# Optimization experiments

Measured on AMD Instinct MI355X. Metric: run time of the kernel, lower is better.

The kernel has to match this reference:

```python
import jax, jax.numpy as jnp
import numpy as np

NUM_KNOTS = 10
DEGREE = 3
NUM_BASIS = NUM_KNOTS + DEGREE - 1  # 12
IN_FEATURES = 512
OUT_FEATURES = 512


def _interval_bounds():
    # t = linspace(0,1,num_knots); segment i covers [t[max(0,i-deg+1)], t[min(i+1,K-1)])
    t = np.linspace(0.0, 1.0, NUM_KNOTS, dtype=np.float32)
    idx = np.arange(NUM_BASIS)
    lower = t[np.maximum(0, idx - (DEGREE - 1))]
    upper = t[np.minimum(idx + 1, NUM_KNOTS - 1)]
    return jnp.asarray(lower), jnp.asarray(upper)


def setup_inputs() -> dict:
    key = jax.random.key(0)
    kx, kc = jax.random.split(key)
    x = jax.random.uniform(kx, (8, 2048, IN_FEATURES), dtype=jnp.float32)
    # coeffs for spline (i=out, j=in): torch indexes splines[i*in_features+j]
    coeffs = jax.random.normal(kc, (OUT_FEATURES, IN_FEATURES, NUM_BASIS), dtype=jnp.float32)
    return {"x": x, "coeffs": coeffs}


def reference(x, coeffs):
    lower, upper = _interval_bounds()  # [NUM_BASIS] each
    # piecewise-constant basis masks: [b, s, in, NUM_BASIS]
    xe = x[..., None]
    basis = ((xe >= lower) & (xe < upper)).astype(x.dtype)
    # out[b,s,i] = sum_j sum_k basis[b,s,j,k] * coeffs[i,j,k]
    return jnp.einsum("bsjk,ijk->bsi", basis, coeffs)
```

## Files before the change

### kernel.cpp

```cpp
#include <hip/hip_runtime.h>

#define MTOT 16384
#define NFEAT 512
#define KTOT 4608

typedef float f32x16 __attribute__((ext_vector_type(16)));
typedef short s16x8 __attribute__((ext_vector_type(8)));

__device__ __forceinline__ int div9(int c) { return (c * 7282) >> 16; }

#define GLDS(GP, LP) __builtin_amdgcn_global_load_lds( \
    (const __attribute__((address_space(1))) void*)(GP), \
    (__attribute__((address_space(3))) void*)(LP), 16, 0, 0)

__device__ __forceinline__ s16x8 decode_mask(unsigned msk) {
  unsigned e0 = (msk & 15u) * 0x00204081u & 0x01010101u;
  unsigned e1 = (msk >> 4)  * 0x00204081u & 0x01010101u;
  unsigned d0 = __builtin_amdgcn_perm(e0, e0, 0x0C010C00u) * 0x3F80u;
  unsigned d1 = __builtin_amdgcn_perm(e0, e0, 0x0C030C02u) * 0x3F80u;
  unsigned d2 = __builtin_amdgcn_perm(e1, e1, 0x0C010C00u) * 0x3F80u;
  unsigned d3 = __builtin_amdgcn_perm(e1, e1, 0x0C030C02u) * 0x3F80u;
  union { unsigned d[4]; s16x8 v; } u;
  u.d[0] = d0; u.d[1] = d1; u.d[2] = d2; u.d[3] = d3;
  return u.v;
}

__global__ __launch_bounds__(256) void prep(const float* __restrict__ x,
                                            const float* __restrict__ coeffs,
                                            unsigned char* __restrict__ codeT,
                                            unsigned short* __restrict__ Bmat) {
  __shared__ unsigned char segt[64][68];
  const int bx = blockIdx.x;
  const int tid = threadIdx.x;
  if (bx < 2048) {
    const int i = bx >> 2, q = bx & 3;
    const float* cb = coeffs + (size_t)i * 6144;
#pragma unroll
    for (int p = 0; p < 5; ++p) {
      int kl = p * 256 + tid;
      if (kl < 1152) {
        int k = q * 1152 + kl;
        int j = div9(k), s = k - j * 9;
        float v = cb[j * 12 + s] + cb[j * 12 + s + 1] + cb[j * 12 + s + 2];
        unsigned u = __float_as_uint(v);
        unsigned rn = (u + 0x7FFFu + ((u >> 16) & 1u)) >> 16;
        Bmat[(size_t)i * KTOT + k] = (unsigned short)rn;
      }
    }
  } else {
    const int bb = bx - 2048;
    const int mt = bb >> 3;
    const int jt = bb & 7;
    const int m0 = mt * 64;
    const float4* x4 = (const float4*)x;
    const float T1 = (float)(1.0/9.0), T2 = (float)(2.0/9.0), T3 = (float)(3.0/9.0),
                T4 = (float)(4.0/9.0), T5 = (float)(5.0/9.0), T6 = (float)(6.0/9.0),
                T7 = (float)(7.0/9.0), T8 = (float)(8.0/9.0);
#pragma unroll
    for (int it = 0; it < 4; ++it) {
      int f = it * 256 + tid;
      int m = f >> 4, jq = f & 15;
      float4 v = x4[(size_t)(m0 + m) * 128 + jt * 16 + jq];
      uchar4 sv;
      { float xv = v.x; sv.x = (unsigned char)((xv>=T1)+(xv>=T2)+(xv>=T3)+(xv>=T4)+(xv>=T5)+(xv>=T6)+(xv>=T7)+(xv>=T8)); }
      { float xv = v.y; sv.y = (unsigned char)((xv>=T1)+(xv>=T2)+(xv>=T3)+(xv>=T4)+(xv>=T5)+(xv>=T6)+(xv>=T7)+(xv>=T8)); }
      { float xv = v.z; sv.z = (unsigned char)((xv>=T1)+(xv>=T2)+(xv>=T3)+(xv>=T4)+(xv>=T5)+(xv>=T6)+(xv>=T7)+(xv>=T8)); }
      { float xv = v.w; sv.w = (unsigned char)((xv>=T1)+(xv>=T2)+(xv>=T3)+(xv>=T4)+(xv>=T5)+(xv>=T6)+(xv>=T7)+(xv>=T8)); }
      *(uchar4*)&segt[m][jq * 4] = sv;
    }
    __syncthreads();
#pragma unroll
    for (int p = 0; p < 5; ++p) {
      int u = p * 256 + tid;
      if (u < 1152) {
        int gl = u >> 4, mq = u & 15;
        int c0 = jt * 576 + gl * 8;
        int j0 = div9(c0), j1 = div9(c0 + 7);
        int j0l = j0 - jt * 64, j1l = j1 - jt * 64;
        uchar4 ob;
        unsigned char* pb = (unsigned char*)&ob;
#pragma unroll
        for (int c = 0; c < 4; ++c) {
          int m = mq * 4 + c;
          int s0 = segt[m][j0l];
          int pos0 = j0 * 9 + s0 - c0;
          unsigned code = (pos0 >= 0 && pos0 < 8) ? (1u << pos0) : 0u;
          if (j1 != j0) {
            int s1 = segt[m][j1l];
            int pos1 = j1 * 9 + s1 - c0;
            if (pos1 < 8) code |= (1u << pos1);
          }
          pb[c] = (unsigned char)code;
        }
        *(uchar4*)(codeT + (size_t)(jt * 72 + gl) * MTOT + m0 + mq * 4) = ob;
      }
    }
  }
}

__global__ __launch_bounds__(256, 2) void kan_gemm(const unsigned char* __restrict__ codeT,
                                                   const unsigned short* __restrict__ Bmat,
                                                   float* __restrict__ out) {
  __shared__ __align__(16) short Blds[2][8 * 512];
  const int tid = threadIdx.x;
  const int lane = tid & 63;
  const int wid = tid >> 6;
  const int l5 = lane & 31;
  const int lh = lane >> 5;
  const int bx = blockIdx.x;
  const int nt = bx & 7;
  const int mt = bx >> 3;
  const int m0 = mt * 256, n0 = nt * 64;

  const int s0 = 2 * wid, s1 = 2 * wid + 1;
  const unsigned short* gB0 = Bmat + (size_t)(n0 + (s0 >> 2) * 32 + l5) * KTOT + (s0 & 3) * 16 + lh * 8;
  const unsigned short* gB1 = Bmat + (size_t)(n0 + (s1 >> 2) * 32 + l5) * KTOT + (s1 & 3) * 16 + lh * 8;
  const unsigned char* gCk0 = codeT + (size_t)(0 * 2 + lh) * MTOT + m0 + wid * 64 + l5;
  const unsigned char* gCk1 = codeT + (size_t)(1 * 2 + lh) * MTOT + m0 + wid * 64 + l5;
  const unsigned char* gCk2 = codeT + (size_t)(2 * 2 + lh) * MTOT + m0 + wid * 64 + l5;
  const unsigned char* gCk3 = codeT + (size_t)(3 * 2 + lh) * MTOT + m0 + wid * 64 + l5;

  f32x16 acc[2][2] = {};
  unsigned char crA[8], crB[8];

#define LOAD_CR(CR) do { \
    CR[0] = gCk0[0];  CR[4] = gCk0[32]; \
    CR[1] = gCk1[0];  CR[5] = gCk1[32]; \
    CR[2] = gCk2[0];  CR[6] = gCk2[32]; \
    CR[3] = gCk3[0];  CR[7] = gCk3[32]; \
    gCk0 += (size_t)8 * MTOT; gCk1 += (size_t)8 * MTOT; \
    gCk2 += (size_t)8 * MTOT; gCk3 += (size_t)8 * MTOT; } while (0)

#define ISSUE_B(buf) do { \
    GLDS(gB0, &Blds[buf][0] + s0 * 512); \
    GLDS(gB1, &Blds[buf][0] + s1 * 512); \
    gB0 += 64; gB1 += 64; } while (0)

#define COMPUTE(CR, buf) do { \
    _Pragma("unroll") \
    for (int ks = 0; ks < 4; ++ks) { \
      s16x8 b0 = *(const s16x8*)&Blds[buf][(0 * 4 + ks) * 512 + lane * 8]; \
      s16x8 b1 = *(const s16x8*)&Blds[buf][(1 * 4 + ks) * 512 + lane * 8]; \
      _Pragma("unroll") \
      for (int ms = 0; ms < 2; ++ms) { \
        s16x8 a = decode_mask(CR[ms * 4 + ks]); \
        acc[ms][0] = __builtin_amdgcn_mfma_f32_32x32x16_bf16(a, b0, acc[ms][0], 0, 0, 0); \
        acc[ms][1] = __builtin_amdgcn_mfma_f32_32x32x16_bf16(a, b1, acc[ms][1], 0, 0, 0); \
      } \
    } } while (0)

  LOAD_CR(crA);
  ISSUE_B(0);
  LOAD_CR(crB);
  __syncthreads();

#pragma unroll 1
  for (int kt = 0; kt < 72; kt += 2) {
    ISSUE_B(1);
    COMPUTE(crA, 0);
    if (kt < 70) LOAD_CR(crA);
    __syncthreads();
    if (kt < 70) ISSUE_B(0);
    COMPUTE(crB, 1);
    if (kt < 70) LOAD_CR(crB);
    __syncthreads();
  }

#pragma unroll
  for (int ms = 0; ms < 2; ++ms) {
#pragma unroll
    for (int ns = 0; ns < 2; ++ns) {
      int rowbase = m0 + wid * 64 + ms * 32 + 4 * lh;
      int col = n0 + ns * 32 + l5;
      float* op = out + (size_t)rowbase * NFEAT + col;
#pragma unroll
      for (int rg = 0; rg < 16; ++rg) {
        int row_off = (rg & 3) + 8 * (rg >> 2);
        op[(size_t)row_off * NFEAT] = acc[ms][ns][rg];
      }
    }
  }
}

extern "C" void kernel_launch(void* const* d_in, const int* in_sizes, int n_in,
                              void* d_out, int out_size, void* d_ws, size_t ws_size,
                              hipStream_t stream) {
  const float* x = (const float*)d_in[0];
  const float* coeffs = (const float*)d_in[1];
  float* out = (float*)d_out;
  unsigned char* codeT = (unsigned char*)d_ws;
  unsigned short* Bmat = (unsigned short*)((char*)d_ws + (size_t)576 * MTOT);

  prep<<<dim3(4096), dim3(256), 0, stream>>>(x, coeffs, codeT, Bmat);
  kan_gemm<<<dim3(512), dim3(256), 0, stream>>>(codeT, Bmat, out);
}
```

Measured before the change: 173.3 us.

## Load B fragments straight into registers and retile blocks along N

The shared-memory staging of B and its per-step block barriers are removed. Each wave now loads its own 64-column bf16 B fragments directly from global memory into a double-buffered register set. The block tile changes from 256 rows by 64 columns to 64 rows by 256 columns, so the four waves share the same row codes and each takes a different column slice. This drops LDS traffic and __syncthreads, but raises the B bytes fetched from L2 by about fourfold, uses uncoalesced 16-byte per-row loads, and adds register pressure.

```diff
diff --git a/kernel.cpp b/kernel.cpp
--- a/kernel.cpp
+++ b/kernel.cpp
@@ -8,10 +8,6 @@
 typedef short s16x8 __attribute__((ext_vector_type(8)));
 
 __device__ __forceinline__ int div9(int c) { return (c * 7282) >> 16; }
-
-#define GLDS(GP, LP) __builtin_amdgcn_global_load_lds( \
-    (const __attribute__((address_space(1))) void*)(GP), \
-    (__attribute__((address_space(3))) void*)(LP), 16, 0, 0)
 
 __device__ __forceinline__ s16x8 decode_mask(unsigned msk) {
   unsigned e0 = (msk & 15u) * 0x00204081u & 0x01010101u;
@@ -101,27 +97,35 @@
 __global__ __launch_bounds__(256, 2) void kan_gemm(const unsigned char* __restrict__ codeT,
                                                    const unsigned short* __restrict__ Bmat,
                                                    float* __restrict__ out) {
-  __shared__ __align__(16) short Blds[2][8 * 512];
   const int tid = threadIdx.x;
   const int lane = tid & 63;
   const int wid = tid >> 6;
   const int l5 = lane & 31;
   const int lh = lane >> 5;
   const int bx = blockIdx.x;
-  const int nt = bx & 7;
-  const int mt = bx >> 3;
-  const int m0 = mt * 256, n0 = nt * 64;
+  const int ntb = bx & 1;
+  const int mt = bx >> 1;
+  const int m0 = mt * 64;
+  const int n0w = ntb * 256 + wid * 64;
 
-  const int s0 = 2 * wid, s1 = 2 * wid + 1;
-  const unsigned short* gB0 = Bmat + (size_t)(n0 + (s0 >> 2) * 32 + l5) * KTOT + (s0 & 3) * 16 + lh * 8;
-  const unsigned short* gB1 = Bmat + (size_t)(n0 + (s1 >> 2) * 32 + l5) * KTOT + (s1 & 3) * 16 + lh * 8;
-  const unsigned char* gCk0 = codeT + (size_t)(0 * 2 + lh) * MTOT + m0 + wid * 64 + l5;
-  const unsigned char* gCk1 = codeT + (size_t)(1 * 2 + lh) * MTOT + m0 + wid * 64 + l5;
-  const unsigned char* gCk2 = codeT + (size_t)(2 * 2 + lh) * MTOT + m0 + wid * 64 + l5;
-  const unsigned char* gCk3 = codeT + (size_t)(3 * 2 + lh) * MTOT + m0 + wid * 64 + l5;
+  const unsigned short* gB0 = Bmat + (size_t)(n0w + l5) * KTOT + lh * 8;
+  const unsigned short* gB1 = Bmat + (size_t)(n0w + 32 + l5) * KTOT + lh * 8;
+  const unsigned char* gCk0 = codeT + (size_t)(0 * 2 + lh) * MTOT + m0 + l5;
+  const unsigned char* gCk1 = codeT + (size_t)(1 * 2 + lh) * MTOT + m0 + l5;
+  const unsigned char* gCk2 = codeT + (size_t)(2 * 2 + lh) * MTOT + m0 + l5;
+  const unsigned char* gCk3 = codeT + (size_t)(3 * 2 + lh) * MTOT + m0 + l5;
 
   f32x16 acc[2][2] = {};
+  s16x8 bA[8], bB[8];
   unsigned char crA[8], crB[8];
+
+#define LOAD_B(BX) do { \
+    _Pragma("unroll") \
+    for (int ks = 0; ks < 4; ++ks) { \
+      BX[ks]     = *(const s16x8*)(gB0 + ks * 16); \
+      BX[4 + ks] = *(const s16x8*)(gB1 + ks * 16); \
+    } \
+    gB0 += 64; gB1 += 64; } while (0)
 
 #define LOAD_CR(CR) do { \
     CR[0] = gCk0[0];  CR[4] = gCk0[32]; \
@@ -131,47 +135,34 @@
     gCk0 += (size_t)8 * MTOT; gCk1 += (size_t)8 * MTOT; \
     gCk2 += (size_t)8 * MTOT; gCk3 += (size_t)8 * MTOT; } while (0)
 
-#define ISSUE_B(buf) do { \
-    GLDS(gB0, &Blds[buf][0] + s0 * 512); \
-    GLDS(gB1, &Blds[buf][0] + s1 * 512); \
-    gB0 += 64; gB1 += 64; } while (0)
-
-#define COMPUTE(CR, buf) do { \
+#define COMPUTE(BX, CR) do { \
     _Pragma("unroll") \
     for (int ks = 0; ks < 4; ++ks) { \
-      s16x8 b0 = *(const s16x8*)&Blds[buf][(0 * 4 + ks) * 512 + lane * 8]; \
-      s16x8 b1 = *(const s16x8*)&Blds[buf][(1 * 4 + ks) * 512 + lane * 8]; \
       _Pragma("unroll") \
       for (int ms = 0; ms < 2; ++ms) { \
         s16x8 a = decode_mask(CR[ms * 4 + ks]); \
-        acc[ms][0] = __builtin_amdgcn_mfma_f32_32x32x16_bf16(a, b0, acc[ms][0], 0, 0, 0); \
-        acc[ms][1] = __builtin_amdgcn_mfma_f32_32x32x16_bf16(a, b1, acc[ms][1], 0, 0, 0); \
+        acc[ms][0] = __builtin_amdgcn_mfma_f32_32x32x16_bf16(a, BX[ks],     acc[ms][0], 0, 0, 0); \
+        acc[ms][1] = __builtin_amdgcn_mfma_f32_32x32x16_bf16(a, BX[4 + ks], acc[ms][1], 0, 0, 0); \
       } \
     } } while (0)
 
-  LOAD_CR(crA);
-  ISSUE_B(0);
-  LOAD_CR(crB);
-  __syncthreads();
+  LOAD_B(bA); LOAD_CR(crA);
+  LOAD_B(bB); LOAD_CR(crB);
 
 #pragma unroll 1
   for (int kt = 0; kt < 72; kt += 2) {
-    ISSUE_B(1);
-    COMPUTE(crA, 0);
-    if (kt < 70) LOAD_CR(crA);
-    __syncthreads();
-    if (kt < 70) ISSUE_B(0);
-    COMPUTE(crB, 1);
-    if (kt < 70) LOAD_CR(crB);
-    __syncthreads();
+    COMPUTE(bA, crA);
+    if (kt < 70) { LOAD_B(bA); LOAD_CR(crA); }
+    COMPUTE(bB, crB);
+    if (kt < 70) { LOAD_B(bB); LOAD_CR(crB); }
   }
 
 #pragma unroll
   for (int ms = 0; ms < 2; ++ms) {
 #pragma unroll
     for (int ns = 0; ns < 2; ++ns) {
-      int rowbase = m0 + wid * 64 + ms * 32 + 4 * lh;
-      int col = n0 + ns * 32 + l5;
+      int rowbase = m0 + ms * 32 + 4 * lh;
+      int col = n0w + ns * 32 + l5;
       float* op = out + (size_t)rowbase * NFEAT + col;
 #pragma unroll
       for (int rg = 0; rg < 16; ++rg) {
```

After: 244.0 us. 40.8% more time.

## Pack mask codes into 64-bit words and retile GEMM to 128-row blocks

Applied to the files above, without the earlier changes.

The prep kernel now packs eight 8-bit basis-mask codes per row into one 64-bit word, so the GEMM loads two 64-bit values per K-step instead of many scattered byte loads. The GEMM tile shrinks from 256 to 128 rows (1024 blocks), and each wave now owns 32 rows with two accumulators instead of four. It also loads a 128-wide K slice of B per stage and raises the occupancy hint to 4 blocks per CU. The aim is fewer, wider code loads and better latency hiding through more resident waves. In exchange, each B tile is reused across fewer rows, so B traffic per output row doubles.

```diff
diff --git a/kernel.cpp b/kernel.cpp
--- a/kernel.cpp
+++ b/kernel.cpp
@@ -27,7 +27,7 @@
 
 __global__ __launch_bounds__(256) void prep(const float* __restrict__ x,
                                             const float* __restrict__ coeffs,
-                                            unsigned char* __restrict__ codeT,
+                                            unsigned long long* __restrict__ codeP,
                                             unsigned short* __restrict__ Bmat) {
   __shared__ unsigned char segt[64][68];
   const int bx = blockIdx.x;
@@ -70,83 +70,81 @@
     }
     __syncthreads();
 #pragma unroll
-    for (int p = 0; p < 5; ++p) {
+    for (int p = 0; p < 3; ++p) {
       int u = p * 256 + tid;
-      if (u < 1152) {
-        int gl = u >> 4, mq = u & 15;
-        int c0 = jt * 576 + gl * 8;
-        int j0 = div9(c0), j1 = div9(c0 + 7);
-        int j0l = j0 - jt * 64, j1l = j1 - jt * 64;
-        uchar4 ob;
-        unsigned char* pb = (unsigned char*)&ob;
+      if (u < 576) {
+        int t = u >> 6, m = u & 63;
+        unsigned long long w = 0ull;
 #pragma unroll
-        for (int c = 0; c < 4; ++c) {
-          int m = mq * 4 + c;
-          int s0 = segt[m][j0l];
+        for (int b = 0; b < 8; ++b) {
+          int gl = t * 8 + b;
+          int c0 = jt * 576 + gl * 8;
+          int j0 = div9(c0), j1 = div9(c0 + 7);
+          int s0 = segt[m][j0 - jt * 64];
           int pos0 = j0 * 9 + s0 - c0;
           unsigned code = (pos0 >= 0 && pos0 < 8) ? (1u << pos0) : 0u;
           if (j1 != j0) {
-            int s1 = segt[m][j1l];
+            int s1 = segt[m][j1 - jt * 64];
             int pos1 = j1 * 9 + s1 - c0;
             if (pos1 < 8) code |= (1u << pos1);
           }
-          pb[c] = (unsigned char)code;
+          w |= (unsigned long long)code << (8 * b);
         }
-        *(uchar4*)(codeT + (size_t)(jt * 72 + gl) * MTOT + m0 + mq * 4) = ob;
+        codeP[(size_t)(jt * 9 + t) * MTOT + m0 + m] = w;
       }
     }
   }
 }
 
-__global__ __launch_bounds__(256, 2) void kan_gemm(const unsigned char* __restrict__ codeT,
+__global__ __launch_bounds__(256, 4) void kan_gemm(const unsigned long long* __restrict__ codeP,
                                                    const unsigned short* __restrict__ Bmat,
                                                    float* __restrict__ out) {
-  __shared__ __align__(16) short Blds[2][8 * 512];
+  __shared__ __align__(16) short Blds[2][8192];
   const int tid = threadIdx.x;
   const int lane = tid & 63;
   const int wid = tid >> 6;
   const int l5 = lane & 31;
   const int lh = lane >> 5;
+  const int lh8 = lh * 8;
   const int bx = blockIdx.x;
   const int nt = bx & 7;
   const int mt = bx >> 3;
-  const int m0 = mt * 256, n0 = nt * 64;
+  const int m0 = mt * 128, n0 = nt * 64;
 
-  const int s0 = 2 * wid, s1 = 2 * wid + 1;
-  const unsigned short* gB0 = Bmat + (size_t)(n0 + (s0 >> 2) * 32 + l5) * KTOT + (s0 & 3) * 16 + lh * 8;
-  const unsigned short* gB1 = Bmat + (size_t)(n0 + (s1 >> 2) * 32 + l5) * KTOT + (s1 & 3) * 16 + lh * 8;
-  const unsigned char* gCk0 = codeT + (size_t)(0 * 2 + lh) * MTOT + m0 + wid * 64 + l5;
-  const unsigned char* gCk1 = codeT + (size_t)(1 * 2 + lh) * MTOT + m0 + wid * 64 + l5;
-  const unsigned char* gCk2 = codeT + (size_t)(2 * 2 + lh) * MTOT + m0 + wid * 64 + l5;
-  const unsigned char* gCk3 = codeT + (size_t)(3 * 2 + lh) * MTOT + m0 + wid * 64 + l5;
+  const unsigned short* gB[4];
+#pragma unroll
+  for (int q = 0; q < 4; ++q) {
+    int s = wid * 4 + q, ns = s >> 3, ksl = s & 7;
+    gB[q] = Bmat + (size_t)(n0 + ns * 32 + l5) * KTOT + ksl * 16 + lh * 8;
+  }
+  const unsigned long long* gC = codeP + m0 + wid * 32 + l5;
 
-  f32x16 acc[2][2] = {};
-  unsigned char crA[8], crB[8];
+  f32x16 acc[2] = {};
+  unsigned crA[4], crB[4];
 
 #define LOAD_CR(CR) do { \
-    CR[0] = gCk0[0];  CR[4] = gCk0[32]; \
-    CR[1] = gCk1[0];  CR[5] = gCk1[32]; \
-    CR[2] = gCk2[0];  CR[6] = gCk2[32]; \
-    CR[3] = gCk3[0];  CR[7] = gCk3[32]; \
-    gCk0 += (size_t)8 * MTOT; gCk1 += (size_t)8 * MTOT; \
-    gCk2 += (size_t)8 * MTOT; gCk3 += (size_t)8 * MTOT; } while (0)
+    unsigned long long a = gC[0], b = gC[MTOT]; \
+    CR[0] = (unsigned)a; CR[1] = (unsigned)(a >> 32); \
+    CR[2] = (unsigned)b; CR[3] = (unsigned)(b >> 32); \
+    gC += (size_t)2 * MTOT; } while (0)
 
 #define ISSUE_B(buf) do { \
-    GLDS(gB0, &Blds[buf][0] + s0 * 512); \
-    GLDS(gB1, &Blds[buf][0] + s1 * 512); \
-    gB0 += 64; gB1 += 64; } while (0)
+    _Pragma("unroll") \
+    for (int q = 0; q < 4; ++q) { \
+      GLDS(gB[q], &Blds[buf][0] + (wid * 4 + q) * 512 + lane * 8); \
+      gB[q] += 128; \
+    } } while (0)
 
-#define COMPUTE(CR, buf) do { \
+#define COMPUTE(buf, CR) do { \
     _Pragma("unroll") \
-    for (int ks = 0; ks < 4; ++ks) { \
-      s16x8 b0 = *(const s16x8*)&Blds[buf][(0 * 4 + ks) * 512 + lane * 8]; \
-      s16x8 b1 = *(const s16x8*)&Blds[buf][(1 * 4 + ks) * 512 + lane * 8]; \
-      _Pragma("unroll") \
-      for (int ms = 0; ms < 2; ++ms) { \
-        s16x8 a = decode_mask(CR[ms * 4 + ks]); \
-        acc[ms][0] = __builtin_amdgcn_mfma_f32_32x32x16_bf16(a, b0, acc[ms][0], 0, 0, 0); \
-        acc[ms][1] = __builtin_amdgcn_mfma_f32_32x32x16_bf16(a, b1, acc[ms][1], 0, 0, 0); \
-      } \
+    for (int ks = 0; ks < 8; ++ks) { \
+      unsigned wrd = CR[((ks >> 2) << 1) | ((ks >> 1) & 1)]; \
+      unsigned msk = ((wrd >> ((ks & 1) * 16)) >> lh8) & 0xFFu; \
+      s16x8 a = decode_mask(msk); \
+      s16x8 b0 = *(const s16x8*)&Blds[buf][ks * 512 + lane * 8]; \
+      s16x8 b1 = *(const s16x8*)&Blds[buf][(8 + ks) * 512 + lane * 8]; \
+      acc[0] = __builtin_amdgcn_mfma_f32_32x32x16_bf16(a, b0, acc[0], 0, 0, 0); \
+      acc[1] = __builtin_amdgcn_mfma_f32_32x32x16_bf16(a, b1, acc[1], 0, 0, 0); \
     } } while (0)
 
   LOAD_CR(crA);
@@ -155,29 +153,26 @@
   __syncthreads();
 
 #pragma unroll 1
-  for (int kt = 0; kt < 72; kt += 2) {
+  for (int p = 0; p < 36; p += 2) {
     ISSUE_B(1);
-    COMPUTE(crA, 0);
-    if (kt < 70) LOAD_CR(crA);
+    COMPUTE(0, crA);
+    if (p < 34) LOAD_CR(crA);
     __syncthreads();
-    if (kt < 70) ISSUE_B(0);
-    COMPUTE(crB, 1);
-    if (kt < 70) LOAD_CR(crB);
+    if (p < 34) ISSUE_B(0);
+    COMPUTE(1, crB);
+    if (p < 34) LOAD_CR(crB);
     __syncthreads();
   }
 
 #pragma unroll
-  for (int ms = 0; ms < 2; ++ms) {
+  for (int ns = 0; ns < 2; ++ns) {
+    int rowbase = m0 + wid * 32 + 4 * lh;
+    int col = n0 + ns * 32 + l5;
+    float* op = out + (size_t)rowbase * NFEAT + col;
 #pragma unroll
-    for (int ns = 0; ns < 2; ++ns) {
-      int rowbase = m0 + wid * 64 + ms * 32 + 4 * lh;
-      int col = n0 + ns * 32 + l5;
-      float* op = out + (size_t)rowbase * NFEAT + col;
-#pragma unroll
-      for (int rg = 0; rg < 16; ++rg) {
-        int row_off = (rg & 3) + 8 * (rg >> 2);
-        op[(size_t)row_off * NFEAT] = acc[ms][ns][rg];
-      }
+    for (int rg = 0; rg < 16; ++rg) {
+      int row_off = (rg & 3) + 8 * (rg >> 2);
+      op[(size_t)row_off * NFEAT] = acc[ns][rg];
     }
   }
 }
@@ -188,9 +183,9 @@
   const float* x = (const float*)d_in[0];
   const float* coeffs = (const float*)d_in[1];
   float* out = (float*)d_out;
-  unsigned char* codeT = (unsigned char*)d_ws;
-  unsigned short* Bmat = (unsigned short*)((char*)d_ws + (size_t)576 * MTOT);
+  unsigned long long* codeP = (unsigned long long*)d_ws;
+  unsigned short* Bmat = (unsigned short*)((char*)d_ws + (size_t)72 * MTOT * 8);
 
-  prep<<<dim3(4096), dim3(256), 0, stream>>>(x, coeffs, codeT, Bmat);
-  kan_gemm<<<dim3(512), dim3(256), 0, stream>>>(codeT, Bmat, out);
+  prep<<<dim3(4096), dim3(256), 0, stream>>>(x, coeffs, codeP, Bmat);
+  kan_gemm<<<dim3(1024), dim3(256), 0, stream>>>(codeP, Bmat, out);
 }
```

After: 178.8 us. 1.03x slower.
